# Performance work log

Measured on AMD Instinct MI355X. Metric: run time of the kernel, lower is better.

The kernel has to match this reference:

```python
import math
import jax, jax.numpy as jnp
import numpy as np

B, S, DIM = 4, 2048, 1024
N_HEADS = 16
HEAD_DIM = DIM // N_HEADS  # 64
THETA = 10000.0


def _rope_tables(seq_len):
    # theta_of_dims = 1/theta^(2i/head_dim) for i in 0..head_dim/2
    inv = 1.0 / (THETA ** (jnp.arange(0, HEAD_DIM, 2, dtype=jnp.float32) / HEAD_DIM))
    pos = jnp.arange(seq_len, dtype=jnp.float32)[:, None]
    freqs = pos * inv  # [S, HEAD_DIM/2]
    return jnp.cos(freqs), jnp.sin(freqs)


def _apply_rope(x, cos, sin):
    # x: [B, S, H, HEAD_DIM]; complex pairs are (even, odd) interleaved
    xr = x[..., 0::2]
    xi = x[..., 1::2]
    c = cos[None, :, None, :]  # [1, S, 1, HEAD_DIM/2]
    s = sin[None, :, None, :]
    out_r = xr * c - xi * s
    out_i = xr * s + xi * c
    return jnp.stack([out_r, out_i], axis=-1).reshape(x.shape)


def setup_inputs() -> dict:
    key = jax.random.key(0)
    kx, kl, kq, kk, kv, ko = jax.random.split(key, 6)
    scale = 0.02
    return {
        "x": jax.random.normal(kx, (B, S, DIM), dtype=jnp.float32),
        "seq_lens": jax.random.randint(kl, (B,), 1, S, dtype=jnp.int32),
        "wq": jax.random.normal(kq, (DIM, DIM), dtype=jnp.float32) * scale,
        "wk": jax.random.normal(kk, (DIM, DIM), dtype=jnp.float32) * scale,
        "wv": jax.random.normal(kv, (DIM, DIM), dtype=jnp.float32) * scale,
        "wo": jax.random.normal(ko, (DIM, DIM), dtype=jnp.float32) * scale,
    }


def reference(x, seq_lens, wq, wk, wv, wo):
    b, s, _ = x.shape
    # padding mask: mask[idx, :l, l:] = -inf (rows < l cannot attend to cols >= l)
    pos = jnp.arange(s)
    l = seq_lens[:, None, None]  # [B,1,1]
    mask = jnp.where((pos[None, :, None] < l) & (pos[None, None, :] >= l),
                     -jnp.inf, 0.0).astype(jnp.float32)  # [B,S,S]

    xq = (x @ wq.T).reshape(b, s, N_HEADS, HEAD_DIM)
    xk = (x @ wk.T).reshape(b, s, N_HEADS, HEAD_DIM)
    xv = (x @ wv.T).reshape(b, s, N_HEADS, HEAD_DIM)

    cos, sin = _rope_tables(s)
    xq = _apply_rope(xq, cos, sin)
    xk = _apply_rope(xk, cos, sin)

    q = xq.transpose(0, 2, 1, 3)  # [B,H,S,D]
    k = xk.transpose(0, 2, 1, 3)
    v = xv.transpose(0, 2, 1, 3)

    scores = jnp.einsum('bhqd,bhkd->bhqk', q, k) / math.sqrt(HEAD_DIM)
    scores = scores + mask[:, None, :, :]
    probs = jax.nn.softmax(scores, axis=-1)
    out = jnp.einsum('bhqk,bhkd->bhqd', probs, v)  # [B,H,S,D]
    out = out.transpose(0, 2, 1, 3).reshape(b, s, DIM)
    return out @ wo.T
```

## Files before the change

### kernel.cpp

```cpp
#include <hip/hip_runtime.h>
#include <hip/hip_bf16.h>
#include <stdint.h>


typedef __attribute__((ext_vector_type(8))) short s8v;
typedef __attribute__((ext_vector_type(2))) float f2v;
typedef __attribute__((ext_vector_type(4))) float f4v;
typedef __attribute__((ext_vector_type(16))) float f16v;

#define GLL16(gsrc, ldst) __builtin_amdgcn_global_load_lds(              \
    (const __attribute__((address_space(1))) void*)(gsrc),               \
    (__attribute__((address_space(3))) void*)(ldst), 16, 0, 0)

__device__ __forceinline__ short f2bf(float f) {
  union { float f; unsigned i; } v; v.f = f;
  unsigned r = v.i + 0x7fffu + ((v.i >> 16) & 1u);
  return (short)(r >> 16);
}
__device__ __forceinline__ unsigned cvtpk(float a, float b) {
  unsigned r;
  asm("v_cvt_pk_bf16_f32 %0, %1, %2" : "=v"(r) : "v"(a), "v"(b));
  return r;
}
__device__ __forceinline__ void plswap(unsigned& x, unsigned& y) {
  asm volatile("v_permlane32_swap_b32 %0, %1" : "+v"(x), "+v"(y));
}

__global__ __launch_bounds__(256) void k_prep(
    const float* __restrict__ x,
    const float* __restrict__ wq, const float* __restrict__ wk,
    const float* __restrict__ wv, const float* __restrict__ wo,
    float* __restrict__ ct, float* __restrict__ st,
    short* __restrict__ xb, short* __restrict__ wqkv, short* __restrict__ wob)
{
  int id = blockIdx.x * 256 + threadIdx.x;
  if (id < 65536) {
    const int pos = id >> 5, i = id & 31;
    float inv = exp2f(-13.287712379549449f * ((float)i / 32.0f));
    float a = (float)pos * inv;
    float s, c;
    sincosf(a, &s, &c);
    ct[id] = c; st[id] = s;
    return;
  }
  id -= 65536;
  if (id < 2097152) {
    float4 v = ((const float4*)x)[id];
    short4 o;
    o.x = f2bf(v.x); o.y = f2bf(v.y); o.z = f2bf(v.z); o.w = f2bf(v.w);
    ((short4*)xb)[id] = o;
    return;
  }
  id -= 2097152;
  const int sel = id >> 18;
  const int off = id & 262143;
  const float* src = (sel == 0) ? wq : (sel == 1) ? wk : (sel == 2) ? wv : wo;
  short* dst = (sel < 3) ? (wqkv + (size_t)sel * 1048576) : wob;
  float4 v = ((const float4*)src)[off];
  short4 o;
  o.x = f2bf(v.x); o.y = f2bf(v.y); o.z = f2bf(v.z); o.w = f2bf(v.w);
  ((short4*)dst)[off] = o;
}

__global__ __launch_bounds__(256, 2) void k_gemm_qkv(
    const short* __restrict__ xb, const short* __restrict__ wb,
    const float* __restrict__ ct, const float* __restrict__ st,
    short* __restrict__ qb, short* __restrict__ kb, short* __restrict__ vt)
{
  __shared__ short As[2][128 * 64];
  __shared__ short Bs[2][128 * 64];
  const int bid = blockIdx.x;
  const int item = (bid & 7) * 192 + (bid >> 3);
  const int row_m = (item & 63) * 128;
  const int row_n = (item >> 6) * 128;
  const int tid = threadIdx.x;
  const int lane = tid & 63, w = tid >> 6;
  const int g = lane >> 4, lq = lane & 15;
  const int wm = (w >> 1) * 64, wn = (w & 1) * 64;
  const int srow = tid >> 3;
  const int schunk = (lane & 7) ^ ((lane >> 3) & 7);

  f4v acc[4][4];
#pragma unroll
  for (int i = 0; i < 4; i++)
#pragma unroll
    for (int j = 0; j < 4; j++) acc[i][j] = f4v{0.f, 0.f, 0.f, 0.f};

  auto stage = [&](int kt, int s) {
#pragma unroll
    for (int j = 0; j < 4; j++)
      GLL16(xb + (size_t)(row_m + j * 32 + srow) * 1024 + kt + schunk * 8,
            &As[s][j * 2048 + w * 512]);
#pragma unroll
    for (int j = 0; j < 4; j++)
      GLL16(wb + (size_t)(row_n + j * 32 + srow) * 1024 + kt + schunk * 8,
            &Bs[s][j * 2048 + w * 512]);
  };

  stage(0, 0);
  stage(64, 1);
  asm volatile("s_waitcnt vmcnt(8)" ::: "memory");
  __builtin_amdgcn_sched_barrier(0);
  asm volatile("s_barrier" ::: "memory");

  for (int t = 0; t < 16; t++) {
    const int s = t & 1;
    const short* Ac = &As[s][0];
    const short* Bc = &Bs[s][0];
#pragma unroll
    for (int kk = 0; kk < 2; kk++) {
      s8v a[4], b[4];
#pragma unroll
      for (int mi = 0; mi < 4; mi++) {
        const int r_ = wm + mi * 16 + lq;
        a[mi] = *(const s8v*)&Ac[r_ * 64 + (((kk * 4 + g) ^ (lq & 7)) * 8)];
      }
#pragma unroll
      for (int ni = 0; ni < 4; ni++) {
        const int r_ = wn + ni * 16 + lq;
        b[ni] = *(const s8v*)&Bc[r_ * 64 + (((kk * 4 + g) ^ (lq & 7)) * 8)];
      }
      __builtin_amdgcn_s_setprio(1);
#pragma unroll
      for (int mi = 0; mi < 4; mi++)
#pragma unroll
        for (int ni = 0; ni < 4; ni++)
          acc[mi][ni] = __builtin_amdgcn_mfma_f32_16x16x32_bf16(a[mi], b[ni], acc[mi][ni], 0, 0, 0);
      __builtin_amdgcn_s_setprio(0);
    }
    if (t < 15) {
      asm volatile("s_waitcnt lgkmcnt(0)" ::: "memory");
      asm volatile("s_barrier" ::: "memory");
      if (t < 14) {
        stage((t + 2) * 64, s);
        asm volatile("s_waitcnt vmcnt(8)" ::: "memory");
      } else {
        asm volatile("s_waitcnt vmcnt(0)" ::: "memory");
      }
      __builtin_amdgcn_sched_barrier(0);
      asm volatile("s_barrier" ::: "memory");
    }
  }

  const int sel = row_n >> 10;
  if (sel < 2) {
    const float qsc = (sel == 0) ? 0.18033688011112042f : 1.0f;
    short* __restrict__ dst = (sel == 0) ? qb : kb;
#pragma unroll
    for (int mi = 0; mi < 4; mi++) {
#pragma unroll
      for (int ni = 0; ni < 4; ni++) {
        const int o = row_n + wn + ni * 16 + lq;
        const int oin = o & 1023, h = oin >> 6, d = oin & 63;
#pragma unroll
        for (int r = 0; r < 4; r++) {
          const int tt = row_m + wm + mi * 16 + g * 4 + r;
          const int b_ = tt >> 11, s_ = tt & 2047;
          float v = acc[mi][ni][r];
          float p = __shfl_xor(v, 1);
          const int i2 = d >> 1;
          const float cv = ct[s_ * 32 + i2], sv = st[s_ * 32 + i2];
          float outv = (d & 1) ? fmaf(p, sv, v * cv) : fmaf(-p, sv, v * cv);
          dst[((size_t)(b_ * 16 + h) * 2048 + s_) * 64 + d] = f2bf(outv * qsc);
        }
      }
    }
  } else {
#pragma unroll
    for (int mi = 0; mi < 4; mi++) {
#pragma unroll
      for (int ni = 0; ni < 4; ni++) {
        const int o = row_n + wn + ni * 16 + lq;
        const int oin = o & 1023, h = oin >> 6, d = oin & 63;
        const int t0 = row_m + wm + mi * 16 + g * 4;
        const int b_ = t0 >> 11, s_ = t0 & 2047;
        short4 pk;
        pk.x = f2bf(acc[mi][ni][0]); pk.y = f2bf(acc[mi][ni][1]);
        pk.z = f2bf(acc[mi][ni][2]); pk.w = f2bf(acc[mi][ni][3]);
        *(short4*)&vt[((size_t)(b_ * 16 + h) * 64 + d) * 2048 + s_] = pk;
      }
    }
  }
}

__global__ __launch_bounds__(256, 3) void k_attn(
    const short* __restrict__ qb, const short* __restrict__ kb, const short* __restrict__ vt,
    const int* __restrict__ seq_lens, short* __restrict__ ao)
{
  __shared__ short KV[24576];
  const int n = blockIdx.x;
  const int m = n >> 3;
  const int bh = (n & 7) * 8 + (m & 7);
  const int qblk = m >> 3;
  const int b = bh >> 4, h = bh & 15;
  const int tid = threadIdx.x, lane = tid & 63, w = tid >> 6;
  const int lq32 = lane & 31, hl = lane >> 5;
  const int L = seq_lens[b];
  const int q0 = qblk * 128 + w * 32;
  const int lr = lane >> 3, sc = (lane & 7) ^ (lr & 7);

  const short* kbase = kb + (size_t)bh * 2048 * 64;
  const short* vbase = vt + (size_t)bh * 64 * 2048;

  const short* qsrc = qb + ((size_t)bh * 2048 + q0 + lq32) * 64 + 8 * hl;
  s8v qf[4];
#pragma unroll
  for (int ki = 0; ki < 4; ki++) qf[ki] = *(const s8v*)&qsrc[16 * ki];

  f2v lacc[8];
#pragma unroll
  for (int i = 0; i < 8; i++) lacc[i] = f2v{0.f, 0.f};
  f16v O[2];
  O[0] = f16v{0.f,0.f,0.f,0.f,0.f,0.f,0.f,0.f,0.f,0.f,0.f,0.f,0.f,0.f,0.f,0.f};
  O[1] = O[0];

  const bool blk_below = (qblk * 128 + 127) < L;
  const int nt = (blk_below ? ((L + 63) & ~63) : 2048) >> 6;
  const bool wave_below = (q0 + 31) < L;
  const int qp = q0 + lq32;
  const int rsw = (lq32 & 7);

  auto stage = [&](int tile, int slot) {
    const int tn = tile * 64;
#pragma unroll
    for (int i = 0; i < 2; i++) {
      const int c = w * 2 + i;
      GLL16(kbase + (size_t)(tn + c * 8 + lr) * 64 + sc * 8, &KV[slot * 4096 + c * 512]);
      GLL16(vbase + (size_t)(c * 8 + lr) * 2048 + tn + sc * 8, &KV[12288 + slot * 4096 + c * 512]);
    }
  };

  stage(0, 0);
  if (nt > 1) stage(1, 1);

  int sl = 0;
  for (int t = 0; t < nt; t++) {
    if (t + 1 < nt) {
      asm volatile("s_waitcnt vmcnt(4)" ::: "memory");
    } else {
      asm volatile("s_waitcnt vmcnt(0)" ::: "memory");
    }
    __builtin_amdgcn_sched_barrier(0);
    asm volatile("s_barrier" ::: "memory");

    if (t + 2 < nt) {
      int sn = sl + 2; if (sn >= 3) sn -= 3;
      stage(t + 2, sn);
    }

    const int t0 = t * 64;
    if (!(wave_below && t0 >= L)) {
      const short* Kc = &KV[sl * 4096];
      const short* Vc = &KV[12288 + sl * 4096];

      f16v sa[2];
      __builtin_amdgcn_s_setprio(1);
#pragma unroll
      for (int sub = 0; sub < 2; sub++) {
        f16v acc = f16v{0.f,0.f,0.f,0.f,0.f,0.f,0.f,0.f,0.f,0.f,0.f,0.f,0.f,0.f,0.f,0.f};
#pragma unroll
        for (int ki = 0; ki < 4; ki++) {
          s8v kf = *(const s8v*)&Kc[(sub * 32 + lq32) * 64 + (((2 * ki + hl) ^ rsw) * 8)];
          acc = __builtin_amdgcn_mfma_f32_32x32x16_bf16(kf, qf[ki], acc, 0, 0, 0);
        }
        sa[sub] = acc;
      }
      __builtin_amdgcn_s_setprio(0);

      const bool nomask = (t0 + 64 <= L) || (q0 >= L);
      if (!nomask) {
        const bool qfree = (qp >= L);
#pragma unroll
        for (int sub = 0; sub < 2; sub++)
#pragma unroll
          for (int r = 0; r < 16; r++) {
            const int kvp = t0 + sub * 32 + (r & 3) + 8 * (r >> 2) + 4 * hl;
            if (!(qfree || kvp < L)) sa[sub][r] = -1e30f;
          }
      }

#pragma unroll
      for (int sub = 0; sub < 2; sub++)
#pragma unroll
        for (int r = 0; r < 16; r++)
          sa[sub][r] = __builtin_amdgcn_exp2f(sa[sub][r]);
#pragma unroll
      for (int r8 = 0; r8 < 8; r8++) {
        f2v a = f2v{sa[0][2 * r8], sa[0][2 * r8 + 1]};
        f2v c = f2v{sa[1][2 * r8], sa[1][2 * r8 + 1]};
        lacc[r8] += a + c;
      }

      __builtin_amdgcn_s_setprio(1);
#pragma unroll
      for (int sub = 0; sub < 2; sub++) {
        unsigned c0 = cvtpk(sa[sub][0],  sa[sub][1]);
        unsigned c1 = cvtpk(sa[sub][2],  sa[sub][3]);
        unsigned c2 = cvtpk(sa[sub][4],  sa[sub][5]);
        unsigned c3 = cvtpk(sa[sub][6],  sa[sub][7]);
        plswap(c0, c2);
        plswap(c1, c3);
        unsigned c4 = cvtpk(sa[sub][8],  sa[sub][9]);
        unsigned c5 = cvtpk(sa[sub][10], sa[sub][11]);
        unsigned c6 = cvtpk(sa[sub][12], sa[sub][13]);
        unsigned c7 = cvtpk(sa[sub][14], sa[sub][15]);
        plswap(c4, c6);
        plswap(c5, c7);
        union P8 { unsigned u[4]; s8v s; };
        P8 pa, pb;
        pa.u[0] = c0; pa.u[1] = c1; pa.u[2] = c2; pa.u[3] = c3;
        pb.u[0] = c4; pb.u[1] = c5; pb.u[2] = c6; pb.u[3] = c7;
#pragma unroll
        for (int dt = 0; dt < 2; dt++) {
          s8v vf0 = *(const s8v*)&Vc[(32 * dt + lq32) * 64 + (((4 * sub + hl) ^ rsw) * 8)];
          O[dt] = __builtin_amdgcn_mfma_f32_32x32x16_bf16(vf0, pa.s, O[dt], 0, 0, 0);
          s8v vf1 = *(const s8v*)&Vc[(32 * dt + lq32) * 64 + (((4 * sub + 2 + hl) ^ rsw) * 8)];
          O[dt] = __builtin_amdgcn_mfma_f32_32x32x16_bf16(vf1, pb.s, O[dt], 0, 0, 0);
        }
      }
      __builtin_amdgcn_s_setprio(0);
    }
    if (++sl == 3) sl = 0;
  }

  f2v l2 = (lacc[0] + lacc[1]) + (lacc[2] + lacc[3]);
  f2v l3 = (lacc[4] + lacc[5]) + (lacc[6] + lacc[7]);
  l2 += l3;
  float l_run = l2.x + l2.y;
  l_run += __shfl_xor(l_run, 32);
  const float inv = 1.0f / l_run;
  asm volatile("s_barrier" ::: "memory");
  short* es = &KV[w * 2048];
#pragma unroll
  for (int dt = 0; dt < 2; dt++)
#pragma unroll
    for (int rp = 0; rp < 8; rp++) {
      unsigned u = cvtpk(O[dt][2 * rp] * inv, O[dt][2 * rp + 1] * inv);
      const int col = 32 * dt + 8 * (rp >> 1) + 2 * (rp & 1) + 4 * hl;
      const int chunk = col >> 3, within = col & 7;
      *(unsigned*)&es[lq32 * 64 + ((chunk ^ (lq32 & 7)) << 3) + within] = u;
    }
  asm volatile("" ::: "memory");
#pragma unroll
  for (int pph = 0; pph < 4; pph++) {
    const int qq = pph * 8 + lr;
    const int ch = lane & 7;
    s8v vv = *(const s8v*)&es[qq * 64 + ((ch ^ lr) << 3)];
    *(s8v*)&ao[((size_t)b * 2048 + q0 + qq) * 1024 + h * 64 + ch * 8] = vv;
  }
}

__global__ __launch_bounds__(256, 2) void k_gemm_out(
    const short* __restrict__ ab, const short* __restrict__ wob, float* __restrict__ out)
{
  __shared__ short As[2][128 * 64];
  __shared__ short Bs[2][128 * 64];
  const int bid = blockIdx.x;
  const int item = (bid & 7) * 64 + (bid >> 3);
  const int row_m = (item & 63) * 128;
  const int row_n = (item >> 6) * 128;
  const int tid = threadIdx.x;
  const int lane = tid & 63, w = tid >> 6;
  const int g = lane >> 4, lq = lane & 15;
  const int wm = (w >> 1) * 64, wn = (w & 1) * 64;
  const int srow = tid >> 3;
  const int schunk = (lane & 7) ^ ((lane >> 3) & 7);

  f4v acc[4][4];
#pragma unroll
  for (int i = 0; i < 4; i++)
#pragma unroll
    for (int j = 0; j < 4; j++) acc[i][j] = f4v{0.f, 0.f, 0.f, 0.f};

  auto stage = [&](int kt, int s) {
#pragma unroll
    for (int j = 0; j < 4; j++)
      GLL16(ab + (size_t)(row_m + j * 32 + srow) * 1024 + kt + schunk * 8,
            &As[s][j * 2048 + w * 512]);
#pragma unroll
    for (int j = 0; j < 4; j++)
      GLL16(wob + (size_t)(row_n + j * 32 + srow) * 1024 + kt + schunk * 8,
            &Bs[s][j * 2048 + w * 512]);
  };

  stage(0, 0);
  stage(64, 1);
  asm volatile("s_waitcnt vmcnt(8)" ::: "memory");
  __builtin_amdgcn_sched_barrier(0);
  asm volatile("s_barrier" ::: "memory");

  for (int t = 0; t < 16; t++) {
    const int s = t & 1;
    const short* Ac = &As[s][0];
    const short* Bc = &Bs[s][0];
#pragma unroll
    for (int kk = 0; kk < 2; kk++) {
      s8v a[4], b[4];
#pragma unroll
      for (int mi = 0; mi < 4; mi++) {
        const int r_ = wm + mi * 16 + lq;
        a[mi] = *(const s8v*)&Ac[r_ * 64 + (((kk * 4 + g) ^ (lq & 7)) * 8)];
      }
#pragma unroll
      for (int ni = 0; ni < 4; ni++) {
        const int r_ = wn + ni * 16 + lq;
        b[ni] = *(const s8v*)&Bc[r_ * 64 + (((kk * 4 + g) ^ (lq & 7)) * 8)];
      }
      __builtin_amdgcn_s_setprio(1);
#pragma unroll
      for (int mi = 0; mi < 4; mi++)
#pragma unroll
        for (int ni = 0; ni < 4; ni++)
          acc[mi][ni] = __builtin_amdgcn_mfma_f32_16x16x32_bf16(a[mi], b[ni], acc[mi][ni], 0, 0, 0);
      __builtin_amdgcn_s_setprio(0);
    }
    if (t < 15) {
      asm volatile("s_waitcnt lgkmcnt(0)" ::: "memory");
      asm volatile("s_barrier" ::: "memory");
      if (t < 14) {
        stage((t + 2) * 64, s);
        asm volatile("s_waitcnt vmcnt(8)" ::: "memory");
      } else {
        asm volatile("s_waitcnt vmcnt(0)" ::: "memory");
      }
      __builtin_amdgcn_sched_barrier(0);
      asm volatile("s_barrier" ::: "memory");
    }
  }

#pragma unroll
  for (int mi = 0; mi < 4; mi++)
#pragma unroll
    for (int ni = 0; ni < 4; ni++) {
      const int o = row_n + wn + ni * 16 + lq;
#pragma unroll
      for (int r = 0; r < 4; r++) {
        const int tt = row_m + wm + mi * 16 + g * 4 + r;
        out[(size_t)tt * 1024 + o] = acc[mi][ni][r];
      }
    }
}

extern "C" void kernel_launch(void* const* d_in, const int* in_sizes, int n_in,
                              void* d_out, int out_size, void* d_ws, size_t ws_size,
                              hipStream_t stream) {
  const float* x  = (const float*)d_in[0];
  const int*   sl = (const int*)d_in[1];
  const float* wq = (const float*)d_in[2];
  const float* wk = (const float*)d_in[3];
  const float* wv = (const float*)d_in[4];
  const float* wo = (const float*)d_in[5];
  float* out = (float*)d_out;

  char* ws = (char*)d_ws;
  float* ct   = (float*)(ws + 0);
  float* st   = (float*)(ws + 262144);
  short* xb   = (short*)(ws + 524288);
  short* wqkv = (short*)(ws + 17301504);
  short* wob  = (short*)(ws + 23592960);
  short* qb   = (short*)(ws + 25690112);
  short* kbf  = (short*)(ws + 42467328);
  short* vtb  = (short*)(ws + 76021760);
  short* ab   = (short*)(ws + 92798976);

  k_prep<<<12544, 256, 0, stream>>>(x, wq, wk, wv, wo, ct, st, xb, wqkv, wob);
  k_gemm_qkv<<<1536, 256, 0, stream>>>(xb, wqkv, ct, st, qb, kbf, vtb);
  k_attn<<<1024, 256, 0, stream>>>(qb, kbf, vtb, sl, ab);
  k_gemm_out<<<512, 256, 0, stream>>>(ab, wob, out);
}
```

Baseline: 193.8 us.

## Process two 32-row query sets per wave in attention to reuse K/V tiles

Each attention wave now handles 64 query rows as two 32-row groups that share each staged K/V tile in LDS, and each block covers 256 queries, so the grid is halved. This is meant to halve global-to-LDS K/V traffic and barrier overhead per query. It doubles the accumulator register footprint, which lowers the occupancy target to 2 blocks per CU. Coarser blocks also make the below-length early termination apply less often.

```diff
diff --git a/kernel.cpp b/kernel.cpp
--- a/kernel.cpp
+++ b/kernel.cpp
@@ -183,7 +183,7 @@
   }
 }
 
-__global__ __launch_bounds__(256, 3) void k_attn(
+__global__ __launch_bounds__(256, 2) void k_attn(
     const short* __restrict__ qb, const short* __restrict__ kb, const short* __restrict__ vt,
     const int* __restrict__ seq_lens, short* __restrict__ ao)
 {
@@ -196,28 +196,30 @@
   const int tid = threadIdx.x, lane = tid & 63, w = tid >> 6;
   const int lq32 = lane & 31, hl = lane >> 5;
   const int L = seq_lens[b];
-  const int q0 = qblk * 128 + w * 32;
+  const int q0 = qblk * 256 + w * 64;
   const int lr = lane >> 3, sc = (lane & 7) ^ (lr & 7);
 
   const short* kbase = kb + (size_t)bh * 2048 * 64;
   const short* vbase = vt + (size_t)bh * 64 * 2048;
 
-  const short* qsrc = qb + ((size_t)bh * 2048 + q0 + lq32) * 64 + 8 * hl;
-  s8v qf[4];
-#pragma unroll
-  for (int ki = 0; ki < 4; ki++) qf[ki] = *(const s8v*)&qsrc[16 * ki];
-
-  f2v lacc[8];
-#pragma unroll
-  for (int i = 0; i < 8; i++) lacc[i] = f2v{0.f, 0.f};
-  f16v O[2];
-  O[0] = f16v{0.f,0.f,0.f,0.f,0.f,0.f,0.f,0.f,0.f,0.f,0.f,0.f,0.f,0.f,0.f,0.f};
-  O[1] = O[0];
-
-  const bool blk_below = (qblk * 128 + 127) < L;
+  const short* qsrcA = qb + ((size_t)bh * 2048 + q0 + lq32) * 64 + 8 * hl;
+  const short* qsrcB = qsrcA + 32 * 64;
+  s8v qfA[4], qfB[4];
+#pragma unroll
+  for (int ki = 0; ki < 4; ki++) { qfA[ki] = *(const s8v*)&qsrcA[16 * ki];
+                                   qfB[ki] = *(const s8v*)&qsrcB[16 * ki]; }
+
+  f2v laccA[8], laccB[8];
+#pragma unroll
+  for (int i = 0; i < 8; i++) { laccA[i] = f2v{0.f, 0.f}; laccB[i] = f2v{0.f, 0.f}; }
+  f16v OA[2], OB[2];
+  OA[0] = f16v{0.f,0.f,0.f,0.f,0.f,0.f,0.f,0.f,0.f,0.f,0.f,0.f,0.f,0.f,0.f,0.f};
+  OA[1] = OA[0]; OB[0] = OA[0]; OB[1] = OA[0];
+
+  const bool blk_below = (qblk * 256 + 255) < L;
   const int nt = (blk_below ? ((L + 63) & ~63) : 2048) >> 6;
-  const bool wave_below = (q0 + 31) < L;
-  const int qp = q0 + lq32;
+  const bool belowA = (q0 + 31) < L;
+  const bool belowB = (q0 + 63) < L;
   const int rsw = (lq32 & 7);
 
   auto stage = [&](int tile, int slot) {
@@ -228,6 +230,76 @@
       GLL16(kbase + (size_t)(tn + c * 8 + lr) * 64 + sc * 8, &KV[slot * 4096 + c * 512]);
       GLL16(vbase + (size_t)(c * 8 + lr) * 2048 + tn + sc * 8, &KV[12288 + slot * 4096 + c * 512]);
     }
+  };
+
+  auto process = [&](const s8v (&qf)[4], f16v (&O)[2], f2v (&lacc)[8],
+                     int q0l, const short* Kc, const short* Vc, int t0) {
+    f16v sa[2];
+    __builtin_amdgcn_s_setprio(1);
+#pragma unroll
+    for (int sub = 0; sub < 2; sub++) {
+      f16v acc = f16v{0.f,0.f,0.f,0.f,0.f,0.f,0.f,0.f,0.f,0.f,0.f,0.f,0.f,0.f,0.f,0.f};
+#pragma unroll
+      for (int ki = 0; ki < 4; ki++) {
+        s8v kf = *(const s8v*)&Kc[(sub * 32 + lq32) * 64 + (((2 * ki + hl) ^ rsw) * 8)];
+        acc = __builtin_amdgcn_mfma_f32_32x32x16_bf16(kf, qf[ki], acc, 0, 0, 0);
+      }
+      sa[sub] = acc;
+    }
+    __builtin_amdgcn_s_setprio(0);
+
+    const bool nomask = (t0 + 64 <= L) || (q0l >= L);
+    if (!nomask) {
+      const bool qfree = ((q0l + lq32) >= L);
+#pragma unroll
+      for (int sub = 0; sub < 2; sub++)
+#pragma unroll
+        for (int r = 0; r < 16; r++) {
+          const int kvp = t0 + sub * 32 + (r & 3) + 8 * (r >> 2) + 4 * hl;
+          if (!(qfree || kvp < L)) sa[sub][r] = -1e30f;
+        }
+    }
+
+#pragma unroll
+    for (int sub = 0; sub < 2; sub++)
+#pragma unroll
+      for (int r = 0; r < 16; r++)
+        sa[sub][r] = __builtin_amdgcn_exp2f(sa[sub][r]);
+#pragma unroll
+    for (int r8 = 0; r8 < 8; r8++) {
+      f2v a = f2v{sa[0][2 * r8], sa[0][2 * r8 + 1]};
+      f2v c = f2v{sa[1][2 * r8], sa[1][2 * r8 + 1]};
+      lacc[r8] += a + c;
+    }
+
+    __builtin_amdgcn_s_setprio(1);
+#pragma unroll
+    for (int sub = 0; sub < 2; sub++) {
+      unsigned c0 = cvtpk(sa[sub][0],  sa[sub][1]);
+      unsigned c1 = cvtpk(sa[sub][2],  sa[sub][3]);
+      unsigned c2 = cvtpk(sa[sub][4],  sa[sub][5]);
+      unsigned c3 = cvtpk(sa[sub][6],  sa[sub][7]);
+      plswap(c0, c2);
+      plswap(c1, c3);
+      unsigned c4 = cvtpk(sa[sub][8],  sa[sub][9]);
+      unsigned c5 = cvtpk(sa[sub][10], sa[sub][11]);
+      unsigned c6 = cvtpk(sa[sub][12], sa[sub][13]);
+      unsigned c7 = cvtpk(sa[sub][14], sa[sub][15]);
+      plswap(c4, c6);
+      plswap(c5, c7);
+      union P8 { unsigned u[4]; s8v s; };
+      P8 pa, pb;
+      pa.u[0] = c0; pa.u[1] = c1; pa.u[2] = c2; pa.u[3] = c3;
+      pb.u[0] = c4; pb.u[1] = c5; pb.u[2] = c6; pb.u[3] = c7;
+#pragma unroll
+      for (int dt = 0; dt < 2; dt++) {
+        s8v vf0 = *(const s8v*)&Vc[(32 * dt + lq32) * 64 + (((4 * sub + hl) ^ rsw) * 8)];
+        O[dt] = __builtin_amdgcn_mfma_f32_32x32x16_bf16(vf0, pa.s, O[dt], 0, 0, 0);
+        s8v vf1 = *(const s8v*)&Vc[(32 * dt + lq32) * 64 + (((4 * sub + 2 + hl) ^ rsw) * 8)];
+        O[dt] = __builtin_amdgcn_mfma_f32_32x32x16_bf16(vf1, pb.s, O[dt], 0, 0, 0);
+      }
+    }
+    __builtin_amdgcn_s_setprio(0);
   };
 
   stage(0, 0);
@@ -249,93 +321,35 @@
     }
 
     const int t0 = t * 64;
-    if (!(wave_below && t0 >= L)) {
-      const short* Kc = &KV[sl * 4096];
-      const short* Vc = &KV[12288 + sl * 4096];
-
-      f16v sa[2];
-      __builtin_amdgcn_s_setprio(1);
-#pragma unroll
-      for (int sub = 0; sub < 2; sub++) {
-        f16v acc = f16v{0.f,0.f,0.f,0.f,0.f,0.f,0.f,0.f,0.f,0.f,0.f,0.f,0.f,0.f,0.f,0.f};
-#pragma unroll
-        for (int ki = 0; ki < 4; ki++) {
-          s8v kf = *(const s8v*)&Kc[(sub * 32 + lq32) * 64 + (((2 * ki + hl) ^ rsw) * 8)];
-          acc = __builtin_amdgcn_mfma_f32_32x32x16_bf16(kf, qf[ki], acc, 0, 0, 0);
-        }
-        sa[sub] = acc;
-      }
-      __builtin_amdgcn_s_setprio(0);
-
-      const bool nomask = (t0 + 64 <= L) || (q0 >= L);
-      if (!nomask) {
-        const bool qfree = (qp >= L);
-#pragma unroll
-        for (int sub = 0; sub < 2; sub++)
-#pragma unroll
-          for (int r = 0; r < 16; r++) {
-            const int kvp = t0 + sub * 32 + (r & 3) + 8 * (r >> 2) + 4 * hl;
-            if (!(qfree || kvp < L)) sa[sub][r] = -1e30f;
-          }
-      }
-
-#pragma unroll
-      for (int sub = 0; sub < 2; sub++)
-#pragma unroll
-        for (int r = 0; r < 16; r++)
-          sa[sub][r] = __builtin_amdgcn_exp2f(sa[sub][r]);
-#pragma unroll
-      for (int r8 = 0; r8 < 8; r8++) {
-        f2v a = f2v{sa[0][2 * r8], sa[0][2 * r8 + 1]};
-        f2v c = f2v{sa[1][2 * r8], sa[1][2 * r8 + 1]};
-        lacc[r8] += a + c;
-      }
-
-      __builtin_amdgcn_s_setprio(1);
-#pragma unroll
-      for (int sub = 0; sub < 2; sub++) {
-        unsigned c0 = cvtpk(sa[sub][0],  sa[sub][1]);
-        unsigned c1 = cvtpk(sa[sub][2],  sa[sub][3]);
-        unsigned c2 = cvtpk(sa[sub][4],  sa[sub][5]);
-        unsigned c3 = cvtpk(sa[sub][6],  sa[sub][7]);
-        plswap(c0, c2);
-        plswap(c1, c3);
-        unsigned c4 = cvtpk(sa[sub][8],  sa[sub][9]);
-        unsigned c5 = cvtpk(sa[sub][10], sa[sub][11]);
-        unsigned c6 = cvtpk(sa[sub][12], sa[sub][13]);
-        unsigned c7 = cvtpk(sa[sub][14], sa[sub][15]);
-        plswap(c4, c6);
-        plswap(c5, c7);
-        union P8 { unsigned u[4]; s8v s; };
-        P8 pa, pb;
-        pa.u[0] = c0; pa.u[1] = c1; pa.u[2] = c2; pa.u[3] = c3;
-        pb.u[0] = c4; pb.u[1] = c5; pb.u[2] = c6; pb.u[3] = c7;
-#pragma unroll
-        for (int dt = 0; dt < 2; dt++) {
-          s8v vf0 = *(const s8v*)&Vc[(32 * dt + lq32) * 64 + (((4 * sub + hl) ^ rsw) * 8)];
-          O[dt] = __builtin_amdgcn_mfma_f32_32x32x16_bf16(vf0, pa.s, O[dt], 0, 0, 0);
-          s8v vf1 = *(const s8v*)&Vc[(32 * dt + lq32) * 64 + (((4 * sub + 2 + hl) ^ rsw) * 8)];
-          O[dt] = __builtin_amdgcn_mfma_f32_32x32x16_bf16(vf1, pb.s, O[dt], 0, 0, 0);
-        }
-      }
-      __builtin_amdgcn_s_setprio(0);
-    }
+    const short* Kc = &KV[sl * 4096];
+    const short* Vc = &KV[12288 + sl * 4096];
+    if (!(belowA && t0 >= L)) process(qfA, OA, laccA, q0,      Kc, Vc, t0);
+    if (!(belowB && t0 >= L)) process(qfB, OB, laccB, q0 + 32, Kc, Vc, t0);
+
     if (++sl == 3) sl = 0;
   }
 
-  f2v l2 = (lacc[0] + lacc[1]) + (lacc[2] + lacc[3]);
-  f2v l3 = (lacc[4] + lacc[5]) + (lacc[6] + lacc[7]);
+  f2v l2 = (laccA[0] + laccA[1]) + (laccA[2] + laccA[3]);
+  f2v l3 = (laccA[4] + laccA[5]) + (laccA[6] + laccA[7]);
   l2 += l3;
-  float l_run = l2.x + l2.y;
-  l_run += __shfl_xor(l_run, 32);
-  const float inv = 1.0f / l_run;
+  float lA = l2.x + l2.y;
+  lA += __shfl_xor(lA, 32);
+  const float invA = 1.0f / lA;
+  l2 = (laccB[0] + laccB[1]) + (laccB[2] + laccB[3]);
+  l3 = (laccB[4] + laccB[5]) + (laccB[6] + laccB[7]);
+  l2 += l3;
+  float lB = l2.x + l2.y;
+  lB += __shfl_xor(lB, 32);
+  const float invB = 1.0f / lB;
+
   asm volatile("s_barrier" ::: "memory");
   short* es = &KV[w * 2048];
+
 #pragma unroll
   for (int dt = 0; dt < 2; dt++)
 #pragma unroll
     for (int rp = 0; rp < 8; rp++) {
-      unsigned u = cvtpk(O[dt][2 * rp] * inv, O[dt][2 * rp + 1] * inv);
+      unsigned u = cvtpk(OA[dt][2 * rp] * invA, OA[dt][2 * rp + 1] * invA);
       const int col = 32 * dt + 8 * (rp >> 1) + 2 * (rp & 1) + 4 * hl;
       const int chunk = col >> 3, within = col & 7;
       *(unsigned*)&es[lq32 * 64 + ((chunk ^ (lq32 & 7)) << 3) + within] = u;
@@ -347,6 +361,25 @@
     const int ch = lane & 7;
     s8v vv = *(const s8v*)&es[qq * 64 + ((ch ^ lr) << 3)];
     *(s8v*)&ao[((size_t)b * 2048 + q0 + qq) * 1024 + h * 64 + ch * 8] = vv;
+  }
+  asm volatile("" ::: "memory");
+
+#pragma unroll
+  for (int dt = 0; dt < 2; dt++)
+#pragma unroll
+    for (int rp = 0; rp < 8; rp++) {
+      unsigned u = cvtpk(OB[dt][2 * rp] * invB, OB[dt][2 * rp + 1] * invB);
+      const int col = 32 * dt + 8 * (rp >> 1) + 2 * (rp & 1) + 4 * hl;
+      const int chunk = col >> 3, within = col & 7;
+      *(unsigned*)&es[lq32 * 64 + ((chunk ^ (lq32 & 7)) << 3) + within] = u;
+    }
+  asm volatile("" ::: "memory");
+#pragma unroll
+  for (int pph = 0; pph < 4; pph++) {
+    const int qq = pph * 8 + lr;
+    const int ch = lane & 7;
+    s8v vv = *(const s8v*)&es[qq * 64 + ((ch ^ lr) << 3)];
+    *(s8v*)&ao[((size_t)b * 2048 + q0 + 32 + qq) * 1024 + h * 64 + ch * 8] = vv;
   }
 }
 
@@ -465,6 +498,6 @@
 
   k_prep<<<12544, 256, 0, stream>>>(x, wq, wk, wv, wo, ct, st, xb, wqkv, wob);
   k_gemm_qkv<<<1536, 256, 0, stream>>>(xb, wqkv, ct, st, qb, kbf, vtb);
-  k_attn<<<1024, 256, 0, stream>>>(qb, kbf, vtb, sl, ab);
+  k_attn<<<512, 256, 0, stream>>>(qb, kbf, vtb, sl, ab);
   k_gemm_out<<<512, 256, 0, stream>>>(ab, wob, out);
 }
```

Result: no change. 191.5 us (-1.2%).
